# Performance work log

Measured on AMD Instinct MI355X. Metric: run time of the kernel, lower is better.

Reference implementation:

```python
import jax, jax.numpy as jnp
import numpy as np

H = 450    # hidden_size (JTNN default)
LAT = 56   # latent_size (tree_vec dim)
V = 780    # vocab size
T = 1024   # n_trees
L = 24     # nodes per tree (path topology)


def _tree_meta(Ln):
    # forward edge i: (i, i+1) eid=i ; reverse edge i: (i+1, i) eid=(Ln-1)+i
    n_f = Ln - 1
    eids, preds, srcs, dsts, labels = [], [], [], [], []
    for i in range(n_f):  # forward DFS steps
        eids.append(i); srcs.append(i); dsts.append(i + 1)
        preds.append(i - 1 if i > 0 else -1); labels.append(0)
    for k in range(n_f):  # backtrack DFS steps (reverse edges, deepest first)
        i = n_f - 1 - k
        eids.append(n_f + i); srcs.append(i + 1); dsts.append(i)
        preds.append(n_f + i + 1 if i < n_f - 1 else -1); labels.append(1)
    # incoming edges of the dst node v (for the node 'pull' h = sum of m)
    in1 = [d - 1 if d > 0 else -1 for d in dsts]
    in2 = [n_f + d if d < n_f else -1 for d in dsts]
    meta = [np.asarray(a, np.int32) for a in (eids, preds, srcs, dsts, in1, in2)]
    return meta, np.asarray(labels, np.float32)


def setup_inputs():
    key = jax.random.key(0)
    ks = jax.random.split(key, 12)
    s = 0.05
    return {
        "wid": jax.random.randint(ks[0], (T, L), 0, V, dtype=jnp.int32),
        "tree_vec": jax.random.normal(ks[1], (T, LAT), jnp.float32),
        "emb": jax.random.normal(ks[2], (V, H)) * s,
        "W_w": jax.random.normal(ks[3], (H + LAT, H)) * s, "W_b": jnp.zeros((H,)),
        "U_w": jax.random.normal(ks[4], (2 * H + LAT, H)) * s, "U_b": jnp.zeros((H,)),
        "Wo_w": jax.random.normal(ks[5], (H, V)) * s, "Wo_b": jnp.zeros((V,)),
        "Us_w": jax.random.normal(ks[6], (H, 1)) * s, "Us_b": jnp.zeros((1,)),
        "Wz_w": jax.random.normal(ks[7], (2 * H, H)) * s, "Wz_b": jnp.zeros((H,)),
        "Wr_w": jax.random.normal(ks[8], (H, H)) * s,
        "Ur_w": jax.random.normal(ks[9], (H, H)) * s, "Ur_b": jnp.zeros((H,)),
        "Wh_w": jax.random.normal(ks[10], (2 * H, H)) * s, "Wh_b": jnp.zeros((H,)),
    }


def reference(wid, tree_vec, emb, W_w, W_b, U_w, U_b, Wo_w, Wo_b, Us_w, Us_b,
              Wz_w, Wz_b, Wr_w, Ur_w, Ur_b, Wh_w, Wh_b):
    Tn, Ln = wid.shape
    n_f = Ln - 1
    nE = 2 * n_f
    meta, labels = _tree_meta(Ln)
    xs = tuple(jnp.asarray(a) for a in meta)
    x = emb[wid]                                  # [T, L, H] node features
    m0 = jnp.zeros((Tn, nE, H), x.dtype)
    rm0 = jnp.zeros((Tn, nE, H), x.dtype)

    def step(carry, sx_):
        m, rm = carry
        eid, pred, src, dst, i1, i2 = sx_
        gp = jnp.maximum(pred, 0)
        s = jnp.where(pred >= 0, m[:, gp], 0.0)        # line-graph pull: sum of m
        arm = jnp.where(pred >= 0, rm[:, gp], 0.0)     # accum_rm
        sxn = x[:, src]                                # src_x
        dxn = x[:, dst]                                # dst_x
        z = jax.nn.sigmoid(jnp.concatenate([sxn, s], 1) @ Wz_w + Wz_b)
        mt = jnp.tanh(jnp.concatenate([sxn, arm], 1) @ Wh_w + Wh_b)
        m_new = (1.0 - z) * s + z * mt
        r = jax.nn.sigmoid(dxn @ Wr_w + m_new @ Ur_w + Ur_b)
        m = m.at[:, eid].set(m_new)
        rm = rm.at[:, eid].set(r * m_new)
        # node pull on v: h_v = sum of m over incoming edges (post edge update)
        h_v = (jnp.where(i1 >= 0, m[:, jnp.maximum(i1, 0)], 0.0)
               + jnp.where(i2 >= 0, m[:, jnp.maximum(i2, 0)], 0.0))
        return (m, rm), (h_v, dxn)

    (_, _), (hs, xvs) = jax.lax.scan(step, (m0, rm0), xs)  # [nE, T, H] each

    tv_steps = jnp.broadcast_to(tree_vec, (nE, Tn, LAT))
    p_in = jnp.concatenate([
        jnp.concatenate([x[:, 0], jnp.zeros((Tn, H), x.dtype), tree_vec], 1),
        jnp.concatenate([xvs, hs, tv_steps], -1).reshape(-1, 2 * H + LAT),
    ], 0)
    q_in = jnp.concatenate([
        jnp.concatenate([jnp.zeros((Tn, H), x.dtype), tree_vec], 1),
        jnp.concatenate([hs[:n_f], tv_steps[:n_f]], -1).reshape(-1, H + LAT),
    ], 0)
    p_targets = jnp.concatenate([jnp.repeat(jnp.asarray(1.0 - labels), Tn),
                                 jnp.zeros((Tn,), jnp.float32)])
    q_targets = wid.T.reshape(-1)

    q_logits = jax.nn.relu(q_in @ W_w + W_b) @ Wo_w + Wo_b
    p_logit = (jax.nn.relu(p_in @ U_w + U_b) @ Us_w + Us_b)[:, 0]
    p_loss = jnp.sum(p_targets * jax.nn.softplus(-p_logit)
                     + (1.0 - p_targets) * jax.nn.softplus(p_logit)) / Tn
    logp = jax.nn.log_softmax(q_logits, -1)
    q_loss = -jnp.sum(jnp.take_along_axis(logp, q_targets[:, None], 1)) / Tn
    p_acc = jnp.mean(((p_logit > 0).astype(jnp.int32) == p_targets.astype(jnp.int32)).astype(jnp.float32))
    q_acc = jnp.mean((jnp.argmax(q_logits, 1) == q_targets).astype(jnp.float32))
    return (q_loss, p_loss, q_acc, p_acc)
```

## Files before the change

### kernel.cpp

```cpp
#include <hip/hip_runtime.h>
#include <hip/hip_bf16.h>
#include <math.h>

#define H 450
#define HP 464
#define KP 480
#define LAT 56
#define V 780
#define LW 24
#define NE 46
#define NF 23
#define SLOT (1024*HP)
#define SROWS 2048
#define QROWS (24*1024)
#define PROWS (47*1024)
#define PTGT  (23*1024)
#define QBLK 6144
#define XBSZ ((size_t)QROWS * HP)

typedef __hip_bfloat16 bf16;
typedef __attribute__((ext_vector_type(8))) short short8;
typedef __attribute__((ext_vector_type(4))) float f32x4;

#define MFMA16(a,b,c) __builtin_amdgcn_mfma_f32_16x16x32_bf16(a,b,c,0,0,0)

__device__ __forceinline__ float sigm(float x) { return 1.f / (1.f + __expf(-x)); }
__device__ __forceinline__ float tanh_f(float x) { return 2.f / (1.f + __expf(-2.f * x)) - 1.f; }
__device__ __forceinline__ float toF(bf16 x) { return __bfloat162float(x); }
__device__ __forceinline__ void stV(float* p, float v) { *p = v; }
__device__ __forceinline__ void stV(bf16* p, float v) { *p = __float2bfloat16(v); }
__device__ __forceinline__ short8 ld8(const bf16* p) { return *reinterpret_cast<const short8*>(p); }

__device__ __forceinline__ void gl_lds(const bf16* g, bf16* l) {
    __builtin_amdgcn_global_load_lds(
        (const __attribute__((address_space(1))) void*)g,
        (__attribute__((address_space(3))) void*)l, 16, 0, 0);
}

__device__ __forceinline__ void xcd_decode128(int b, int C, int& row0, int& col0) {
    int rres = b & 7;
    int colt = (b >> 3) % C;
    int g    = b / (8 * C);
    row0 = (rres + 8 * g) * 128;
    col0 = colt * 128;
}

__global__ __launch_bounds__(256)
void make_bt(const float* __restrict__ src, int K, int N, int ld,
             bf16* __restrict__ dst, int npad) {
    int idx = blockIdx.x * 256 + threadIdx.x;
    if (idx >= npad * KP) return;
    int n = idx / KP, k = idx - n * KP;
    float v = (n < N && k < K) ? src[(size_t)k * ld + n] : 0.f;
    dst[idx] = __float2bfloat16(v);
}

__global__ __launch_bounds__(256)
void pack_bias(const float* __restrict__ zb, const float* __restrict__ hb,
               const float* __restrict__ rb, float* __restrict__ bias4) {
    int i = blockIdx.x * 256 + threadIdx.x;
    if (i >= 1856) return;
    float v = 0.f;
    if (i < 450)       v = zb[i];
    else if (i < 900)  v = hb[i - 450];
    else if (i < 1350) v = rb[i - 900];
    bias4[i] = v;
}

__global__ __launch_bounds__(256)
void zero_init(float* __restrict__ out) {
    int i = threadIdx.x;
    if (i < 4) out[i] = 0.f;
}

__global__ __launch_bounds__(256)
void gather_x(const float* __restrict__ emb, const int* __restrict__ wid,
              bf16* __restrict__ x_all) {
    int e = blockIdx.x * 256 + threadIdx.x;
    if (e >= 24 * 1024 * 225) return;
    int row = e / 225, h2 = e - row * 225;
    int t = row >> 10, n = row & 1023;
    int v = wid[n * LW + t];
    float2 x = ((const float2*)(emb + (size_t)v * H))[h2];
    bf16* dst = x_all + (size_t)row * HP + 2 * h2;
    dst[0] = __float2bfloat16(x.x);
    dst[1] = __float2bfloat16(x.y);
}

template<typename TC>
__global__ __launch_bounds__(256)
void gemm128(const bf16* __restrict__ A, int lda,
             const bf16* __restrict__ Bt, int N, int cblk,
             TC* __restrict__ C, int ldc,
             const float* __restrict__ bias,
             const float* __restrict__ addrow, int addld, int relu) {
    __shared__ bf16 As[128 * 32];
    __shared__ bf16 Bs[128 * 32];
    int tid = threadIdx.x;
    int lane = tid & 63, wave = tid >> 6;
    int wx = wave & 1, wy = wave >> 1;
    int lrow = lane & 15, quad = lane >> 4;
    int perm = ((quad + (lrow >> 1)) & 3) * 8;
    int row0, col0;
    xcd_decode128(blockIdx.x, cblk, row0, col0);
    f32x4 acc[4][4] = {};
    for (int k0i = 0; k0i < 15; k0i++) {
        int k0 = k0i * 32;
#pragma unroll
        for (int r = 0; r < 2; r++) {
            int tt = r * 256 + tid;
            int row = tt >> 2, cl = tt & 3;
            int cg = (cl - (row >> 1)) & 3;
            gl_lds(A  + (size_t)(row0 + row) * lda + k0 + cg * 8, As + tt * 8);
            gl_lds(Bt + (size_t)(col0 + row) * KP  + k0 + cg * 8, Bs + tt * 8);
        }
        __syncthreads();
        short8 a[4], b[4];
#pragma unroll
        for (int f = 0; f < 4; f++)
            a[f] = ld8(As + (wy * 64 + f * 16 + lrow) * 32 + perm);
#pragma unroll
        for (int f = 0; f < 4; f++)
            b[f] = ld8(Bs + (wx * 64 + f * 16 + lrow) * 32 + perm);
#pragma unroll
        for (int fi = 0; fi < 4; fi++)
#pragma unroll
            for (int fj = 0; fj < 4; fj++)
                acc[fi][fj] = MFMA16(a[fi], b[fj], acc[fi][fj]);
        __syncthreads();
    }
#pragma unroll
    for (int fi = 0; fi < 4; fi++)
#pragma unroll
        for (int e = 0; e < 4; e++) {
            int r = row0 + wy * 64 + fi * 16 + quad * 4 + e;
#pragma unroll
            for (int fj = 0; fj < 4; fj++) {
                int c = col0 + wx * 64 + fj * 16 + lrow;
                if (c >= N) continue;
                float v = acc[fi][fj][e];
                if (bias) v += bias[c];
                if (addrow) v += addrow[(size_t)(r & 1023) * addld + c];
                if (relu) v = fmaxf(v, 0.f);
                stV(&C[(size_t)r * ldc + c], v);
            }
        }
}

__global__ __launch_bounds__(256)
void gemm128_pre(const bf16* __restrict__ A,
                 const bf16* __restrict__ Bt,
                 bf16* __restrict__ X0,
                 const float* __restrict__ bias4) {
    __shared__ bf16 As[128 * 32];
    __shared__ bf16 Bs[128 * 32];
    int tid = threadIdx.x;
    int lane = tid & 63, wave = tid >> 6;
    int wx = wave & 1, wy = wave >> 1;
    int lrow = lane & 15, quad = lane >> 4;
    int perm = ((quad + (lrow >> 1)) & 3) * 8;
    int row0, col0;
    xcd_decode128(blockIdx.x, 15, row0, col0);
    f32x4 acc[4][4] = {};
    for (int k0i = 0; k0i < 15; k0i++) {
        int k0 = k0i * 32;
#pragma unroll
        for (int r = 0; r < 2; r++) {
            int tt = r * 256 + tid;
            int row = tt >> 2, cl = tt & 3;
            int cg = (cl - (row >> 1)) & 3;
            gl_lds(A  + (size_t)(row0 + row) * HP + k0 + cg * 8, As + tt * 8);
            gl_lds(Bt + (size_t)(col0 + row) * KP + k0 + cg * 8, Bs + tt * 8);
        }
        __syncthreads();
        short8 a[4], b[4];
#pragma unroll
        for (int f = 0; f < 4; f++)
            a[f] = ld8(As + (wy * 64 + f * 16 + lrow) * 32 + perm);
#pragma unroll
        for (int f = 0; f < 4; f++)
            b[f] = ld8(Bs + (wx * 64 + f * 16 + lrow) * 32 + perm);
#pragma unroll
        for (int fi = 0; fi < 4; fi++)
#pragma unroll
            for (int fj = 0; fj < 4; fj++)
                acc[fi][fj] = MFMA16(a[fi], b[fj], acc[fi][fj]);
        __syncthreads();
    }
#pragma unroll
    for (int fi = 0; fi < 4; fi++)
#pragma unroll
        for (int e = 0; e < 4; e++) {
            int r = row0 + wy * 64 + fi * 16 + quad * 4 + e;
#pragma unroll
            for (int fj = 0; fj < 4; fj++) {
                int c = col0 + wx * 64 + fj * 16 + lrow;
                if (c >= 1800) continue;
                int mm = c / 450;
                int cc = c - mm * 450;
                float v = acc[fi][fj][e] + bias4[c];
                X0[(size_t)mm * XBSZ + (size_t)r * HP + cc] = __float2bfloat16(v);
            }
        }
}

__global__ __launch_bounds__(256)
void p_gemm128(const bf16* __restrict__ hs, const bf16* __restrict__ UbT,
               const bf16* __restrict__ XUa, const float* __restrict__ Ptv,
               const float* __restrict__ Us, float* __restrict__ pl) {
    __shared__ bf16 As[128 * 32];
    __shared__ bf16 Bs[128 * 32];
    int tid = threadIdx.x;
    int lane = tid & 63, wave = tid >> 6;
    int wx = wave & 1, wy = wave >> 1;
    int lrow = lane & 15, quad = lane >> 4;
    int perm = ((quad + (lrow >> 1)) & 3) * 8;
    int row0, col0;
    xcd_decode128(blockIdx.x, 4, row0, col0);
    f32x4 acc[4][4] = {};
    for (int k0i = 0; k0i < 15; k0i++) {
        int k0 = k0i * 32;
#pragma unroll
        for (int r = 0; r < 2; r++) {
            int tt = r * 256 + tid;
            int row = tt >> 2, cl = tt & 3;
            int cg = (cl - (row >> 1)) & 3;
            gl_lds(hs  + (size_t)(row0 + row) * HP + k0 + cg * 8, As + tt * 8);
            gl_lds(UbT + (size_t)(col0 + row) * KP + k0 + cg * 8, Bs + tt * 8);
        }
        __syncthreads();
        short8 a[4], b[4];
#pragma unroll
        for (int f = 0; f < 4; f++)
            a[f] = ld8(As + (wy * 64 + f * 16 + lrow) * 32 + perm);
#pragma unroll
        for (int f = 0; f < 4; f++)
            b[f] = ld8(Bs + (wx * 64 + f * 16 + lrow) * 32 + perm);
#pragma unroll
        for (int fi = 0; fi < 4; fi++)
#pragma unroll
            for (int fj = 0; fj < 4; fj++)
                acc[fi][fj] = MFMA16(a[fi], b[fj], acc[fi][fj]);
        __syncthreads();
    }
#pragma unroll
    for (int fi = 0; fi < 4; fi++)
#pragma unroll
        for (int e = 0; e < 4; e++) {
            int r = row0 + wy * 64 + fi * 16 + quad * 4 + e;
            int t = r >> 10, n = r & 1023;
            int dst = (t < 23) ? (t + 1) : (45 - t);
            float part = 0.f;
#pragma unroll
            for (int fj = 0; fj < 4; fj++) {
                int c = col0 + wx * 64 + fj * 16 + lrow;
                if (c < H) {
                    float h = fmaxf(acc[fi][fj][e] + toF(XUa[((size_t)dst * 1024 + n) * HP + c])
                                    + Ptv[(size_t)n * H + c], 0.f);
                    part += h * Us[c];
                }
            }
#pragma unroll
            for (int off = 1; off < 16; off <<= 1)
                part += __shfl_xor(part, off);
            if (lrow == 0) atomicAdd(&pl[1024 + r], part);
        }
}

__global__ __launch_bounds__(256)
void tv_gemm(const float* __restrict__ tv, const float* __restrict__ Wlat,
             const float* __restrict__ bias, float* __restrict__ out) {
    int n = blockIdx.y;
    int c = blockIdx.x * 256 + threadIdx.x;
    __shared__ float tvs[LAT];
    if (threadIdx.x < LAT) tvs[threadIdx.x] = tv[n * LAT + threadIdx.x];
    __syncthreads();
    if (c < H) {
        float a = bias[c];
#pragma unroll 8
        for (int k = 0; k < LAT; k++) a += tvs[k] * Wlat[(size_t)k * H + c];
        out[(size_t)n * H + c] = a;
    }
}

__global__ __launch_bounds__(1024)
void scan_full(bf16* __restrict__ hs,
               const bf16* __restrict__ WzbT, const bf16* __restrict__ WhbT,
               const bf16* __restrict__ UrT,
               const bf16* __restrict__ Xz, const bf16* __restrict__ Xh,
               const bf16* __restrict__ Xr) {
    __shared__ bf16 mnl[2][16][488];
    __shared__ bf16 rml[16][488];
    __shared__ bf16 xzs[16][464];
    __shared__ bf16 xhs[16][464];
    __shared__ bf16 xrs[16][464];
    int tid = threadIdx.x;
    int lane = tid & 63, w = tid >> 6;
    int lrow = lane & 15, quad = lane >> 4;
    int row0 = blockIdx.x * 16;
    bool fwd = row0 < 1024;
    int nb = row0 & 1023;
    int f0 = w, f1 = w + 16;
    bool hasf1 = (f1 < 29);
    int crow = tid / 58, cj = tid - crow * 58;
    bool cok = tid < 928;
    float sreg[2][4];
#pragma unroll
    for (int i = 0; i < 2; i++)
#pragma unroll
        for (int e = 0; e < 4; e++) sreg[i][e] = 0.f;
    for (int i = tid; i < 2 * 16 * 488; i += 1024) ((bf16*)mnl)[i] = __float2bfloat16(0.f);
    for (int i = tid; i < 16 * 488; i += 1024) ((bf16*)rml)[i] = __float2bfloat16(0.f);
    __syncthreads();

    for (int u = 0; u < 23; u++) {
        int cur = u & 1, prev = cur ^ 1;
        int src = fwd ? u : 23 - u;
        int dst = fwd ? (u + 1) : (22 - u);
        if (cok) {
            gl_lds(Xz + ((size_t)src * 1024 + nb + crow) * HP + cj * 8, &xzs[0][0] + tid * 8);
            gl_lds(Xh + ((size_t)src * 1024 + nb + crow) * HP + cj * 8, &xhs[0][0] + tid * 8);
            if (u < 22)
                gl_lds(Xr + ((size_t)dst * 1024 + nb + crow) * HP + cj * 8, &xrs[0][0] + tid * 8);
        }
        f32x4 az[2], ah[2];
#pragma unroll
        for (int i = 0; i < 2; i++) {
            az[i] = (f32x4){0.f, 0.f, 0.f, 0.f};
            ah[i] = (f32x4){0.f, 0.f, 0.f, 0.f};
        }
        if (u > 0) {
            for (int k = 0; k < 15; k++) {
                short8 sA = *reinterpret_cast<const short8*>(&mnl[prev][lrow][k * 32 + quad * 8]);
                short8 rA = *reinterpret_cast<const short8*>(&rml[lrow][k * 32 + quad * 8]);
                {
                    short8 zB = ld8(WzbT + (size_t)(f0 * 16 + lrow) * KP + k * 32 + quad * 8);
                    short8 hB = ld8(WhbT + (size_t)(f0 * 16 + lrow) * KP + k * 32 + quad * 8);
                    az[0] = MFMA16(sA, zB, az[0]);
                    ah[0] = MFMA16(rA, hB, ah[0]);
                }
                if (hasf1) {
                    short8 zB = ld8(WzbT + (size_t)(f1 * 16 + lrow) * KP + k * 32 + quad * 8);
                    short8 hB = ld8(WhbT + (size_t)(f1 * 16 + lrow) * KP + k * 32 + quad * 8);
                    az[1] = MFMA16(sA, zB, az[1]);
                    ah[1] = MFMA16(rA, hB, ah[1]);
                }
            }
        }
        __syncthreads();

#pragma unroll
        for (int i = 0; i < 2; i++) {
            int f = (i == 0) ? f0 : f1;
            if (i == 1 && !hasf1) break;
            int c = f * 16 + lrow;
            if (c < H) {
#pragma unroll
                for (int e = 0; e < 4; e++) {
                    int rl = quad * 4 + e;
                    float zp = az[i][e] + toF(xzs[rl][c]);
                    float hp = ah[i][e] + toF(xhs[rl][c]);
                    float z = sigm(zp), mt = tanh_f(hp);
                    float mn = (1.f - z) * sreg[i][e] + z * mt;
                    sreg[i][e] = mn;
                    mnl[cur][rl][c] = __float2bfloat16(mn);
                }
            }
        }
        __syncthreads();

        {
            bf16* hso = hs + (size_t)(fwd ? u : 23 + u) * SLOT;
            if (cok) {
                float4 v = *reinterpret_cast<const float4*>(&mnl[cur][crow][cj * 8]);
                *reinterpret_cast<float4*>(hso + (size_t)(nb + crow) * HP + cj * 8) = v;
            }
        }

        if (u < 22) {
            f32x4 ar[2];
#pragma unroll
            for (int i = 0; i < 2; i++) ar[i] = (f32x4){0.f, 0.f, 0.f, 0.f};
            for (int k = 0; k < 15; k++) {
                short8 a = *reinterpret_cast<const short8*>(&mnl[cur][lrow][k * 32 + quad * 8]);
                ar[0] = MFMA16(a, ld8(UrT + (size_t)(f0 * 16 + lrow) * KP + k * 32 + quad * 8), ar[0]);
                if (hasf1)
                    ar[1] = MFMA16(a, ld8(UrT + (size_t)(f1 * 16 + lrow) * KP + k * 32 + quad * 8), ar[1]);
            }
#pragma unroll
            for (int i = 0; i < 2; i++) {
                int f = (i == 0) ? f0 : f1;
                if (i == 1 && !hasf1) break;
                int c = f * 16 + lrow;
                if (c < H) {
#pragma unroll
                    for (int e = 0; e < 4; e++) {
                        int rl = quad * 4 + e;
                        float rp = ar[i][e] + toF(xrs[rl][c]);
                        rml[rl][c] = __float2bfloat16(sigm(rp) * toF(mnl[cur][rl][c]));
                    }
                }
            }
            __syncthreads();
        }
    }
}

__global__ __launch_bounds__(256)
void hv_fixup(bf16* __restrict__ hs) {
    int idx = blockIdx.x * 256 + threadIdx.x;
    if (idx >= 22 * SLOT) return;
    int tl = idx / SLOT;
    int rem = idx - tl * SLOT;
    size_t a = (size_t)(23 + tl) * SLOT + rem;
    size_t b = (size_t)(21 - tl) * SLOT + rem;
    hs[a] = __float2bfloat16(toF(hs[a]) + toF(hs[b]));
}

__global__ __launch_bounds__(256)
void q_root(const float* __restrict__ Qtv, bf16* __restrict__ qh) {
    int idx = blockIdx.x * 256 + threadIdx.x;
    if (idx >= 1024 * H) return;
    int n = idx / H, c = idx - n * H;
    qh[(size_t)n * HP + c] = __float2bfloat16(fmaxf(Qtv[idx], 0.f));
}

__global__ __launch_bounds__(256)
void q_reduce(const float* __restrict__ ql, const int* __restrict__ wid,
              float* __restrict__ qred) {
    int wave = threadIdx.x >> 6, lane = threadIdx.x & 63;
    int r = blockIdx.x * 4 + wave;
    int t = r >> 10, n = r & 1023;
    int tgt = wid[n * LW + t];
    const float4* row4 = (const float4*)(ql + (size_t)r * V);
    float m = -3.4e38f, s = 0.f; int mi = 0x7fffffff;
#pragma unroll
    for (int k = 0; k < 4; k++) {
        int c4 = lane + 64 * k;
        if (c4 < 195) {
            float4 v4 = row4[c4];
            float vv[4] = {v4.x, v4.y, v4.z, v4.w};
#pragma unroll
            for (int e = 0; e < 4; e++) {
                float v = vv[e];
                if (v > m) { s = s * __expf(m - v) + 1.f; m = v; mi = c4 * 4 + e; }
                else s += __expf(v - m);
            }
        }
    }
#pragma unroll
    for (int off = 1; off < 64; off <<= 1) {
        float m2 = __shfl_xor(m, off);
        float s2 = __shfl_xor(s, off);
        int   i2 = __shfl_xor(mi, off);
        if (m2 > m || (m2 == m && i2 < mi)) {
            s = s2 + s * __expf(m - m2);
            m = m2; mi = i2;
        } else {
            s = s + s2 * __expf(m2 - m);
        }
    }
    __shared__ float lred[4][2];
    if (lane == 0) {
        float lse = m + logf(s);
        lred[wave][0] = lse - ql[(size_t)r * V + tgt];
        lred[wave][1] = (mi == tgt) ? 1.f : 0.f;
    }
    __syncthreads();
    if (threadIdx.x == 0) {
        qred[blockIdx.x * 2]     = lred[0][0] + lred[1][0] + lred[2][0] + lred[3][0];
        qred[blockIdx.x * 2 + 1] = lred[0][1] + lred[1][1] + lred[2][1] + lred[3][1];
    }
}

__global__ __launch_bounds__(256)
void q_final(const float* __restrict__ qred, float* __restrict__ out) {
    int tid = threadIdx.x;
    float L = 0.f, A = 0.f;
    for (int i = tid; i < QBLK; i += 256) { L += qred[2 * i]; A += qred[2 * i + 1]; }
    __shared__ float s1[256], s2[256];
    s1[tid] = L; s2[tid] = A;
    __syncthreads();
    for (int k = 128; k > 0; k >>= 1) {
        if (tid < k) { s1[tid] += s1[tid + k]; s2[tid] += s2[tid + k]; }
        __syncthreads();
    }
    if (tid == 0) {
        out[0] = s1[0] * (1.f / 1024.f);
        out[2] = s2[0] * (1.f / 24576.f);
    }
}

__global__ __launch_bounds__(256)
void p_init(float* __restrict__ pl, const float* __restrict__ Us_b) {
    int idx = blockIdx.x * 256 + threadIdx.x;
    if (idx < PROWS) pl[idx] = Us_b[0];
}

__global__ __launch_bounds__(256)
void p_root(const bf16* __restrict__ XUa, const float* __restrict__ Ptv,
            const float* __restrict__ Us, float* __restrict__ pl) {
    int n = blockIdx.x;
    int tid = threadIdx.x;
    const bf16* xa = XUa + (size_t)n * HP;
    const float* pt = Ptv + (size_t)n * H;
    float s = 0.f;
    for (int c = tid; c < H; c += 256)
        s += fmaxf(toF(xa[c]) + pt[c], 0.f) * Us[c];
    __shared__ float red[256];
    red[tid] = s;
    __syncthreads();
    for (int k = 128; k > 0; k >>= 1) {
        if (tid < k) red[tid] += red[tid + k];
        __syncthreads();
    }
    if (tid == 0) atomicAdd(&pl[n], red[0]);
}

__global__ __launch_bounds__(256)
void p_final(const float* __restrict__ pl, float* __restrict__ out) {
    int r = blockIdx.x * 256 + threadIdx.x;
    int tid = threadIdx.x;
    float loss = 0.f, acc = 0.f;
    if (r < PROWS) {
        float l = pl[r];
        int tgt = (r < PTGT) ? 1 : 0;
        float x = tgt ? -l : l;
        loss = fmaxf(x, 0.f) + log1pf(expf(-fabsf(x)));
        int pred = (l > 0.f) ? 1 : 0;
        acc = (pred == tgt) ? 1.f : 0.f;
    }
    __shared__ float s1[256], s2[256];
    s1[tid] = loss; s2[tid] = acc;
    __syncthreads();
    for (int k = 128; k > 0; k >>= 1) {
        if (tid < k) { s1[tid] += s1[tid + k]; s2[tid] += s2[tid + k]; }
        __syncthreads();
    }
    if (tid == 0) {
        atomicAdd(&out[1], s1[0] * (1.f / 1024.f));
        atomicAdd(&out[3], s2[0] * (1.f / 48128.f));
    }
}

extern "C" void kernel_launch(void* const* d_in, const int* in_sizes, int n_in,
                              void* d_out, int out_size, void* d_ws, size_t ws_size,
                              hipStream_t stream) {
    const int*   wid  = (const int*)  d_in[0];
    const float* tv   = (const float*)d_in[1];
    const float* emb  = (const float*)d_in[2];
    const float* W_w  = (const float*)d_in[3];
    const float* W_b  = (const float*)d_in[4];
    const float* U_w  = (const float*)d_in[5];
    const float* U_b  = (const float*)d_in[6];
    const float* Wo_w = (const float*)d_in[7];
    const float* Wo_b = (const float*)d_in[8];
    const float* Us_w = (const float*)d_in[9];
    const float* Us_b = (const float*)d_in[10];
    const float* Wz_w = (const float*)d_in[11];
    const float* Wz_b = (const float*)d_in[12];
    const float* Wr_w = (const float*)d_in[13];
    const float* Ur_w = (const float*)d_in[14];
    const float* Ur_b = (const float*)d_in[15];
    const float* Wh_w = (const float*)d_in[16];
    const float* Wh_b = (const float*)d_in[17];
    float* out = (float*)d_out;

    char* base = (char*)d_ws;
    const size_t XBb = XBSZ * 2;
    bf16*  Xz   = (bf16*)(base);
    bf16*  Xh   = (bf16*)(base + XBb);
    bf16*  Xr   = (bf16*)(base + 2 * XBb);
    bf16*  XUa  = (bf16*)(base + 3 * XBb);
    bf16*  hs   = (bf16*)(base + 4 * XBb);
    bf16*  x_all = hs;
    char*  p1   = base + 4 * XBb + (size_t)NE * SLOT * 2;
    float* Qtv  = (float*)p1;               p1 += (size_t)1024 * H * 4;
    float* Ptv  = (float*)p1;               p1 += (size_t)1024 * H * 4;
    float* pl   = (float*)p1;               p1 += (size_t)PROWS * 4;
    float* qred = (float*)p1;               p1 += (size_t)QBLK * 2 * 4;
    float* bias4 = (float*)p1;              p1 += (size_t)1856 * 4;
    bf16*  BT   = (bf16*)p1;
    bf16* BT4   = BT;
    bf16* WzbT  = BT + (size_t)1856 * KP;
    bf16* WhbT  = WzbT + (size_t)512 * KP;
    bf16* UrT   = WhbT + (size_t)512 * KP;
    bf16* UbT   = UrT  + (size_t)512 * KP;
    bf16* WtopT = UbT  + (size_t)512 * KP;
    bf16* WoT   = WtopT + (size_t)512 * KP;
    bf16*  qh = (bf16*)base;
    float* ql = (float*)(base + (size_t)QROWS * HP * 2);

    zero_init<<<1, 256, 0, stream>>>(out);
    int btg = (512 * KP + 255) / 256;
    int btg450 = (450 * KP + 255) / 256;
    make_bt<<<btg450, 256, 0, stream>>>(Wz_w, H, H, H, BT4,                        450);
    make_bt<<<btg450, 256, 0, stream>>>(Wh_w, H, H, H, BT4 + (size_t)450 * KP,     450);
    make_bt<<<btg450, 256, 0, stream>>>(Wr_w, H, H, H, BT4 + (size_t)900 * KP,     450);
    make_bt<<<(506 * KP + 255) / 256, 256, 0, stream>>>(U_w, H, H, H, BT4 + (size_t)1350 * KP, 506);
    pack_bias<<<8, 256, 0, stream>>>(Wz_b, Wh_b, Ur_b, bias4);
    make_bt<<<btg, 256, 0, stream>>>(Wz_w + 450*450,  H, H, H, WzbT, 512);
    make_bt<<<btg, 256, 0, stream>>>(Wh_w + 450*450,  H, H, H, WhbT, 512);
    make_bt<<<btg, 256, 0, stream>>>(Ur_w,            H, H, H, UrT,  512);
    make_bt<<<btg, 256, 0, stream>>>(U_w + 450*450,   H, H, H, UbT,  512);
    make_bt<<<btg, 256, 0, stream>>>(W_w,             H, H, H, WtopT, 512);
    make_bt<<<(896 * KP + 255) / 256, 256, 0, stream>>>(Wo_w, H, V, V, WoT, 896);

    gather_x<<<(24 * 1024 * 225 + 255) / 256, 256, 0, stream>>>(emb, wid, x_all);
    gemm128_pre<<<(QROWS / 128) * 15, 256, 0, stream>>>(x_all, BT4, Xz, bias4);

    tv_gemm<<<dim3(2, 1024), 256, 0, stream>>>(tv, W_w + 450*450, W_b, Qtv);
    tv_gemm<<<dim3(2, 1024), 256, 0, stream>>>(tv, U_w + 900*450, U_b, Ptv);

    scan_full<<<SROWS / 16, 1024, 0, stream>>>(hs, WzbT, WhbT, UrT, Xz, Xh, Xr);
    hv_fixup<<<(22 * SLOT + 255) / 256, 256, 0, stream>>>(hs);

    p_init<<<(PROWS + 255) / 256, 256, 0, stream>>>(pl, Us_b);
    p_root<<<1024, 256, 0, stream>>>(XUa, Ptv, Us_w, pl);
    p_gemm128<<<(PROWS - 1024) / 128 * 4, 256, 0, stream>>>(hs, UbT, XUa, Ptv, Us_w, pl);
    p_final<<<PROWS / 256, 256, 0, stream>>>(pl, out);

    q_root<<<(1024 * H + 255) / 256, 256, 0, stream>>>(Qtv, qh);
    gemm128<bf16><<<(NF * 1024 / 128) * 4, 256, 0, stream>>>(hs, HP, WtopT, H, 4,
                                                             qh + (size_t)1024 * HP, HP,
                                                             (const float*)nullptr, Qtv, H, 1);
    gemm128<float><<<(QROWS / 128) * 7, 256, 0, stream>>>(qh, HP, WoT, V, 7, ql, V,
                                                          Wo_b, (const float*)nullptr, H, 0);
    q_reduce<<<QBLK, 256, 0, stream>>>(ql, wid, qred);
    q_final<<<1, 256, 0, stream>>>(qred, out);

    (void)in_sizes; (void)n_in; (void)out_size; (void)ws_size;
}
```

Baseline: 1.167 ms.

## Merge weight-prep launches and restructure scan loads and state stores

The many make_bt, pack_bias and zero_init launches are replaced by a single prep_w kernel and a pack_misc kernel, which cuts launch overhead. In the scan kernel, the async global-to-LDS loads of the Xz/Xh/Xr gate inputs become register loads that are issued before the MFMA loop and written to LDS after it, so the load latency can overlap compute. Each new hidden state is now stored to global memory directly from the gate loop with scalar bf16 stores, replacing the separate vectorized copy out of LDS. That removes one pass but makes the global writes narrower and less coalesced.

```diff
diff --git a/kernel.cpp b/kernel.cpp
--- a/kernel.cpp
+++ b/kernel.cpp
@@ -17,6 +17,7 @@
 #define PTGT  (23*1024)
 #define QBLK 6144
 #define XBSZ ((size_t)QROWS * HP)
+#define BTROWS 5312
 
 typedef __hip_bfloat16 bf16;
 typedef __attribute__((ext_vector_type(8))) short short8;
@@ -24,7 +25,7 @@
 
 #define MFMA16(a,b,c) __builtin_amdgcn_mfma_f32_16x16x32_bf16(a,b,c,0,0,0)
 
-__device__ __forceinline__ float sigm(float x) { return 1.f / (1.f + __expf(-x)); }
+__device__ __forceinline__ float sigm_f(float x) { return 1.f / (1.f + __expf(-x)); }
 __device__ __forceinline__ float tanh_f(float x) { return 2.f / (1.f + __expf(-2.f * x)) - 1.f; }
 __device__ __forceinline__ float toF(bf16 x) { return __bfloat162float(x); }
 __device__ __forceinline__ void stV(float* p, float v) { *p = v; }
@@ -46,31 +47,41 @@
 }
 
 __global__ __launch_bounds__(256)
-void make_bt(const float* __restrict__ src, int K, int N, int ld,
-             bf16* __restrict__ dst, int npad) {
+void prep_w(const float* __restrict__ Wz, const float* __restrict__ Wh,
+            const float* __restrict__ Wr, const float* __restrict__ Uw,
+            const float* __restrict__ Ww, const float* __restrict__ Wo,
+            const float* __restrict__ Ur, bf16* __restrict__ BT) {
     int idx = blockIdx.x * 256 + threadIdx.x;
-    if (idx >= npad * KP) return;
-    int n = idx / KP, k = idx - n * KP;
-    float v = (n < N && k < K) ? src[(size_t)k * ld + n] : 0.f;
-    dst[idx] = __float2bfloat16(v);
-}
-
-__global__ __launch_bounds__(256)
-void pack_bias(const float* __restrict__ zb, const float* __restrict__ hb,
-               const float* __restrict__ rb, float* __restrict__ bias4) {
+    if (idx >= BTROWS * KP) return;
+    int r = idx / KP, k = idx - r * KP;
+    const float* src; int n; int N = H; int ld = H;
+    if (r < 1856) {
+        if (r < 450)       { src = Wz; n = r; }
+        else if (r < 900)  { src = Wh; n = r - 450; }
+        else if (r < 1350) { src = Wr; n = r - 900; }
+        else               { src = Uw; n = r - 1350; }
+    } else if (r < 2368) { src = Wz + 450 * 450; n = r - 1856; }
+    else if (r < 2880)   { src = Wh + 450 * 450; n = r - 2368; }
+    else if (r < 3392)   { src = Ur;             n = r - 2880; }
+    else if (r < 3904)   { src = Uw + 450 * 450; n = r - 3392; }
+    else if (r < 4416)   { src = Ww;             n = r - 3904; }
+    else                 { src = Wo; n = r - 4416; N = V; ld = V; }
+    float v = (n < N && k < H) ? src[(size_t)k * ld + n] : 0.f;
+    BT[idx] = __float2bfloat16(v);
+}
+
+__global__ __launch_bounds__(256)
+void pack_misc(const float* __restrict__ zb, const float* __restrict__ hb,
+               const float* __restrict__ rb, float* __restrict__ bias4,
+               float* __restrict__ out) {
     int i = blockIdx.x * 256 + threadIdx.x;
+    if (i < 4) out[i] = 0.f;
     if (i >= 1856) return;
     float v = 0.f;
     if (i < 450)       v = zb[i];
     else if (i < 900)  v = hb[i - 450];
     else if (i < 1350) v = rb[i - 900];
     bias4[i] = v;
-}
-
-__global__ __launch_bounds__(256)
-void zero_init(float* __restrict__ out) {
-    int i = threadIdx.x;
-    if (i < 4) out[i] = 0.f;
 }
 
 __global__ __launch_bounds__(256)
@@ -317,11 +328,12 @@
         int cur = u & 1, prev = cur ^ 1;
         int src = fwd ? u : 23 - u;
         int dst = fwd ? (u + 1) : (22 - u);
+        float4 vz, vh, vr;
         if (cok) {
-            gl_lds(Xz + ((size_t)src * 1024 + nb + crow) * HP + cj * 8, &xzs[0][0] + tid * 8);
-            gl_lds(Xh + ((size_t)src * 1024 + nb + crow) * HP + cj * 8, &xhs[0][0] + tid * 8);
+            vz = *reinterpret_cast<const float4*>(Xz + ((size_t)src * 1024 + nb + crow) * HP + cj * 8);
+            vh = *reinterpret_cast<const float4*>(Xh + ((size_t)src * 1024 + nb + crow) * HP + cj * 8);
             if (u < 22)
-                gl_lds(Xr + ((size_t)dst * 1024 + nb + crow) * HP + cj * 8, &xrs[0][0] + tid * 8);
+                vr = *reinterpret_cast<const float4*>(Xr + ((size_t)dst * 1024 + nb + crow) * HP + cj * 8);
         }
         f32x4 az[2], ah[2];
 #pragma unroll
@@ -347,8 +359,16 @@
                 }
             }
         }
-        __syncthreads();
-
+        if (cok) {
+            *reinterpret_cast<float4*>(&xzs[crow][cj * 8]) = vz;
+            *reinterpret_cast<float4*>(&xhs[crow][cj * 8]) = vh;
+            if (u < 22)
+                *reinterpret_cast<float4*>(&xrs[crow][cj * 8]) = vr;
+        }
+        __syncthreads();
+
+        int hsl = fwd ? u : 23 + u;
+        bf16* hso = hs + (size_t)hsl * SLOT;
 #pragma unroll
         for (int i = 0; i < 2; i++) {
             int f = (i == 0) ? f0 : f1;
@@ -358,24 +378,19 @@
 #pragma unroll
                 for (int e = 0; e < 4; e++) {
                     int rl = quad * 4 + e;
+                    int n = (row0 + rl) & 1023;
                     float zp = az[i][e] + toF(xzs[rl][c]);
                     float hp = ah[i][e] + toF(xhs[rl][c]);
-                    float z = sigm(zp), mt = tanh_f(hp);
+                    float z = sigm_f(zp), mt = tanh_f(hp);
                     float mn = (1.f - z) * sreg[i][e] + z * mt;
                     sreg[i][e] = mn;
-                    mnl[cur][rl][c] = __float2bfloat16(mn);
+                    bf16 mb = __float2bfloat16(mn);
+                    mnl[cur][rl][c] = mb;
+                    hso[(size_t)n * HP + c] = mb;
                 }
             }
         }
         __syncthreads();
-
-        {
-            bf16* hso = hs + (size_t)(fwd ? u : 23 + u) * SLOT;
-            if (cok) {
-                float4 v = *reinterpret_cast<const float4*>(&mnl[cur][crow][cj * 8]);
-                *reinterpret_cast<float4*>(hso + (size_t)(nb + crow) * HP + cj * 8) = v;
-            }
-        }
 
         if (u < 22) {
             f32x4 ar[2];
@@ -397,7 +412,7 @@
                     for (int e = 0; e < 4; e++) {
                         int rl = quad * 4 + e;
                         float rp = ar[i][e] + toF(xrs[rl][c]);
-                        rml[rl][c] = __float2bfloat16(sigm(rp) * toF(mnl[cur][rl][c]));
+                        rml[rl][c] = __float2bfloat16(sigm_f(rp) * toF(mnl[cur][rl][c]));
                     }
                 }
             }
@@ -591,20 +606,9 @@
     bf16*  qh = (bf16*)base;
     float* ql = (float*)(base + (size_t)QROWS * HP * 2);
 
-    zero_init<<<1, 256, 0, stream>>>(out);
-    int btg = (512 * KP + 255) / 256;
-    int btg450 = (450 * KP + 255) / 256;
-    make_bt<<<btg450, 256, 0, stream>>>(Wz_w, H, H, H, BT4,                        450);
-    make_bt<<<btg450, 256, 0, stream>>>(Wh_w, H, H, H, BT4 + (size_t)450 * KP,     450);
-    make_bt<<<btg450, 256, 0, stream>>>(Wr_w, H, H, H, BT4 + (size_t)900 * KP,     450);
-    make_bt<<<(506 * KP + 255) / 256, 256, 0, stream>>>(U_w, H, H, H, BT4 + (size_t)1350 * KP, 506);
-    pack_bias<<<8, 256, 0, stream>>>(Wz_b, Wh_b, Ur_b, bias4);
-    make_bt<<<btg, 256, 0, stream>>>(Wz_w + 450*450,  H, H, H, WzbT, 512);
-    make_bt<<<btg, 256, 0, stream>>>(Wh_w + 450*450,  H, H, H, WhbT, 512);
-    make_bt<<<btg, 256, 0, stream>>>(Ur_w,            H, H, H, UrT,  512);
-    make_bt<<<btg, 256, 0, stream>>>(U_w + 450*450,   H, H, H, UbT,  512);
-    make_bt<<<btg, 256, 0, stream>>>(W_w,             H, H, H, WtopT, 512);
-    make_bt<<<(896 * KP + 255) / 256, 256, 0, stream>>>(Wo_w, H, V, V, WoT, 896);
+    pack_misc<<<8, 256, 0, stream>>>(Wz_b, Wh_b, Ur_b, bias4, out);
+    prep_w<<<(BTROWS * KP + 255) / 256, 256, 0, stream>>>(Wz_w, Wh_w, Wr_w, U_w,
+                                                          W_w, Wo_w, Ur_w, BT);
 
     gather_x<<<(24 * 1024 * 225 + 255) / 256, 256, 0, stream>>>(emb, wid, x_all);
     gemm128_pre<<<(QROWS / 128) * 15, 256, 0, stream>>>(x_all, BT4, Xz, bias4);
```

Result: slower. 1.222 ms (+4.7%).
